# Kernel optimization log

Hardware: AMD Instinct MI355X
Metric: run time of the kernel (lower is better)

Reference implementation:

```python
import jax, jax.numpy as jnp
import numpy as np

IMG = 224
RADIUS_CUTS, AZIMUTH_CUTS = 16, 64
N_RADIUS, N_AZIMUTH = 25, 16          # kr1*kr2 = 25, ka^2 = 16
N_R = RADIUS_CUTS * N_RADIUS          # 400 sampled radii
N_A = AZIMUTH_CUTS * N_AZIMUTH        # 1024 sampled azimuths
EMBED_DIM = 96
KR, KA = 5, 4


def sample_grid(dist, H, W):
    """Per-batch polar sampling coordinates for the spherical distortion model.
    dist: (B, 4) polynomial distortion coefficients (module does dist.transpose(1,0)).
    Returns grid (B, N_R, N_A, 2) in grid_sample convention (x=width coord first),
    and theta_max (B,).
    """
    B = dist.shape[0]
    cf = 0.2 + dist.T                      # (4, B), positive odd-poly coefficients
    c = cf[:, :, None]                     # (4, B, 1) for broadcasting
    theta_max = jnp.full((B,), jnp.pi / 2, dtype=dist.dtype)

    def poly(t):                           # odd polynomial r(theta), t: (B, n)
        t2 = t * t
        return t * (c[0] + t2 * (c[1] + t2 * (c[2] + t2 * c[3])))

    # midpoint theta samples in (0, theta_max)
    theta = theta_max[:, None] * (jnp.arange(N_R, dtype=dist.dtype) + 0.5) / N_R  # (B, N_R)
    r = poly(theta) / poly(theta_max[:, None]) * (H * 0.5)                        # (B, N_R) pixels from center

    phi = (2.0 * jnp.pi) * (jnp.arange(N_A, dtype=dist.dtype) + 0.5) / N_A        # (N_A,)
    xc = r[:, :, None] * jnp.cos(phi)      # (B, N_R, N_A)
    yc = r[:, :, None] * jnp.sin(phi)
    # module: out = cat((yc/(W//2), xc/(H//2)), dim=3)
    grid = jnp.stack([yc / (W // 2), xc / (H // 2)], axis=-1)
    return grid, theta_max


def grid_sample_bilinear(img, grid):
    """torch.nn.functional.grid_sample, bilinear, align_corners=True, zeros padding.
    img: (B,C,H,W), grid: (B,Ho,Wo,2) with grid[...,0]=x (width), grid[...,1]=y (height).
    """
    B, C, H, W = img.shape
    gx = (grid[..., 0] + 1.0) * 0.5 * (W - 1)   # align_corners=True mapping
    gy = (grid[..., 1] + 1.0) * 0.5 * (H - 1)
    x0 = jnp.floor(gx); y0 = jnp.floor(gy)
    wx1 = gx - x0; wx0 = 1.0 - wx1
    wy1 = gy - y0; wy0 = 1.0 - wy1

    def corner(xi, yi, w):
        valid = (xi >= 0) & (xi <= W - 1) & (yi >= 0) & (yi <= H - 1)
        xc_ = jnp.clip(xi, 0, W - 1).astype(jnp.int32)
        yc_ = jnp.clip(yi, 0, H - 1).astype(jnp.int32)
        v = jax.vmap(lambda im, yy, xx: im[:, yy, xx])(img, yc_, xc_)  # (B,C,Ho,Wo)
        return v * (w * valid)[:, None, :, :]

    return (corner(x0, y0, wx0 * wy0) + corner(x0 + 1, y0, wx1 * wy0)
            + corner(x0, y0 + 1, wx0 * wy1) + corner(x0 + 1, y0 + 1, wx1 * wy1))


def conv2d(x, w, b, stride):
    y = jax.lax.conv_general_dilated(x, w, window_strides=stride, padding='VALID',
                                     dimension_numbers=('NCHW', 'OIHW', 'NCHW'))
    return y + b[None, :, None, None]


def setup_inputs() -> dict:
    key = jax.random.key(0)
    k = jax.random.split(key, 6)
    x = jax.random.uniform(k[0], (32, 3, IMG, IMG), dtype=jnp.float32)
    dist = jax.random.uniform(k[1], (32, 4), dtype=jnp.float32)
    w1 = jax.random.normal(k[2], (EMBED_DIM, 3, KR, KA), dtype=jnp.float32) * 0.05
    b1 = jnp.zeros((EMBED_DIM,), dtype=jnp.float32)
    w2 = jax.random.normal(k[3], (EMBED_DIM, EMBED_DIM, KR, KA), dtype=jnp.float32) * 0.05
    b2 = jnp.zeros((EMBED_DIM,), dtype=jnp.float32)
    return {"x": x, "dist": dist, "w1": w1, "b1": b1, "w2": w2, "b2": b2}


def reference(x, dist, w1, b1, w2, b2):
    B, C, H, W = x.shape
    grid, theta_max = sample_grid(dist, H, W)          # (B,400,1024,2)
    sampled = grid_sample_bilinear(x, grid)            # (B,3,400,1024)
    t = conv2d(sampled, w1, b1, (KR, KA))              # (B,96,80,256)
    t = conv2d(t, w2, b2, (KR, KA))                    # (B,96,16,64)
    t = t.reshape(B, EMBED_DIM, -1).transpose(0, 2, 1) # (B,1024,96)
    return (t, theta_max)
```

## Files before the change

kernel.cpp:

```cpp
#include <hip/hip_runtime.h>
#include <hip/hip_bf16.h>
#include <math.h>

#define NBATCH 32
#define IMGSZ  224
#define NR     400
#define NA     1024
#define ED     96
#define SROW   256

typedef __attribute__((ext_vector_type(8))) __bf16 bf16x8;
typedef __attribute__((ext_vector_type(8), aligned(8))) __bf16 bf16x8u;
typedef __attribute__((ext_vector_type(4), aligned(8))) __bf16 bf16x4a;
typedef __attribute__((ext_vector_type(4))) __bf16 bf16x4;
typedef __attribute__((ext_vector_type(4))) float f32x4;

union frag_u { struct { bf16x4a lo, hi; } p; bf16x8 v; };


#define PACK_N   (NBATCH*IMGSZ*IMGSZ)
#define PACK_N4  (PACK_N/4)
#define PACK_B   ((PACK_N4 + 255)/256)
#define PREP_N   (ED*ED*20 + 12*64*8 + NBATCH*NR + NA + NBATCH)
#define PREP_B   ((PREP_N + 255)/256)

__global__ __launch_bounds__(256)
void prep_pack_kernel(const float* __restrict__ x,
                      const float* __restrict__ dist,
                      const float* __restrict__ w1,
                      const float* __restrict__ w2,
                      __bf16* __restrict__ xp,
                      float* __restrict__ rtab,
                      float* __restrict__ costab,
                      float* __restrict__ sintab,
                      __bf16* __restrict__ w2f,
                      __bf16* __restrict__ w1f,
                      float* __restrict__ theta_out) {
    const float PI = 3.14159265358979323846f;
    const float SC = 223.0f / 224.0f;
    int bid = blockIdx.x;

    if (bid < PACK_B) {
        int i4 = bid*256 + threadIdx.x;
        if (i4 >= PACK_N4) return;
        int idx = i4 * 4;
        int b  = idx / (IMGSZ*IMGSZ);
        int px = idx - b*(IMGSZ*IMGSZ);
        const float* p = x + (size_t)b*3*IMGSZ*IMGSZ + px;
        f32x4 cr = *(const f32x4*)(p);
        f32x4 cg = *(const f32x4*)(p + IMGSZ*IMGSZ);
        f32x4 cb = *(const f32x4*)(p + 2*IMGSZ*IMGSZ);
        bf16x8 o0, o1;
        o0[0] = (__bf16)cr[0]; o0[1] = (__bf16)cg[0]; o0[2] = (__bf16)cb[0]; o0[3] = (__bf16)0.0f;
        o0[4] = (__bf16)cr[1]; o0[5] = (__bf16)cg[1]; o0[6] = (__bf16)cb[1]; o0[7] = (__bf16)0.0f;
        o1[0] = (__bf16)cr[2]; o1[1] = (__bf16)cg[2]; o1[2] = (__bf16)cb[2]; o1[3] = (__bf16)0.0f;
        o1[4] = (__bf16)cr[3]; o1[5] = (__bf16)cg[3]; o1[6] = (__bf16)cb[3]; o1[7] = (__bf16)0.0f;
        *(bf16x8*)(xp + (size_t)idx*4)     = o0;
        *(bf16x8*)(xp + (size_t)idx*4 + 8) = o1;
        return;
    }

    int idx = (bid - PACK_B)*256 + threadIdx.x;
    if (idx < ED*ED*20) {
        int j    = idx & 7;
        int lane = (idx >> 3) & 63;
        int grp  = idx >> 9;
        int nt   = grp % 6;
        int t    = grp / 6;
        int icb  = t % 3;
        int p    = t / 3;
        int sw   = (((p & 3) + icb) & 1) * 4;
        int oc = nt*16 + (lane & 15);
        int ic = icb*32 + (lane >> 4)*8 + (j ^ sw);
        w2f[idx] = (__bf16)w2[((size_t)(oc*ED + ic)*5 + (p >> 2))*4 + (p & 3)];
    } else if (idx < ED*ED*20 + 12*64*8) {
        int i2   = idx - ED*ED*20;
        int j    = i2 & 7;
        int lane = (i2 >> 3) & 63;
        int grp  = i2 >> 9;
        int ks = grp / 6, ot = grp % 6;
        int oc = ot*16 + (lane & 15);
        int k  = ks*32 + (lane >> 4)*8 + j;
        w1f[i2] = (k < 60) ? (__bf16)w1[oc*60 + k] : (__bf16)0.0f;
    } else if (idx < ED*ED*20 + 12*64*8 + NBATCH*NR) {
        int i2 = idx - ED*ED*20 - 12*64*8;
        int b = i2 / NR, i = i2 % NR;
        float c0 = 0.2f + dist[b*4+0];
        float c1 = 0.2f + dist[b*4+1];
        float c2 = 0.2f + dist[b*4+2];
        float c3 = 0.2f + dist[b*4+3];
        float tmax = 0.5f * PI;
        float t  = tmax * ((float)i + 0.5f) / (float)NR;
        float t2 = t * t;
        float pt = t * (c0 + t2*(c1 + t2*(c2 + t2*c3)));
        float tm2 = tmax * tmax;
        float pm = tmax * (c0 + tm2*(c1 + tm2*(c2 + tm2*c3)));
        rtab[i2] = pt / pm * (0.5f * (float)IMGSZ);
    } else if (idx < ED*ED*20 + 12*64*8 + NBATCH*NR + NA) {
        int j = idx - ED*ED*20 - 12*64*8 - NBATCH*NR;
        float phi = 2.0f * PI * ((float)j + 0.5f) / (float)NA;
        costab[j] = cosf(phi) * SC;
        sintab[j] = sinf(phi) * SC;
    } else if (idx < PREP_N) {
        theta_out[idx - (ED*ED*20 + 12*64*8 + NBATCH*NR + NA)] = 0.5f * PI;
    }
}

__global__ __launch_bounds__(256, 4)
void mega_kernel(const __bf16* __restrict__ xp,
                 const __bf16* __restrict__ w1f_g,
                 const __bf16* __restrict__ w2f,
                 const float* __restrict__ b1,
                 const float* __restrict__ b2,
                 const float* __restrict__ rtab,
                 const float* __restrict__ costab,
                 const float* __restrict__ sintab,
                 float* __restrict__ out) {
    __shared__ __attribute__((aligned(16))) char smem[39936];
    __bf16* s_samp0 = (__bf16*)smem;
    __bf16* s_samp1 = (__bf16*)(smem + 7680);
    __bf16* t1f     = (__bf16*)(smem + 15360);
    __bf16* s_w1f   = (__bf16*)(smem + 27648);
    float*  red     = (float*)smem;

    int tid = threadIdx.x;
    int bid = blockIdx.x;
    int r2 = bid & 15;
    int aq = (bid >> 4) & 3;
    int b  = bid >> 6;
    int wave = tid >> 6, lane = tid & 63, l15 = lane & 15, quad = lane >> 4;

    #pragma unroll
    for (int i = 0; i < 3; ++i)
        *(bf16x8*)(s_w1f + i*2048 + tid*8) = *(const bf16x8*)(w1f_g + i*2048 + tid*8);

    int col = ((lane >> 2) << 4) + wave*4 + (lane & 3);
    int az  = aq*256 + col;
    float sn = sintab[az];
    float cs = costab[az];
    int scol = wave*64 + lane;
    const __bf16* xpb = xp + (size_t)b*IMGSZ*IMGSZ*4;
    const float* rb = rtab + b*NR + r2*25;

    f32x4 acc2[6];
    #pragma unroll
    for (int nt = 0; nt < 6; ++nt) acc2[nt] = (f32x4){0.f,0.f,0.f,0.f};

    auto sample = [&](int kr, __bf16* sb) {
        #pragma unroll
        for (int q = 0; q < 5; ++q) {
            float r  = rb[kr*5 + q];
            float gx = fmaf(r, sn, 111.5f);
            float gy = fmaf(r, cs, 111.5f);
            float x0f = floorf(gx), y0f = floorf(gy);
            float wx1 = gx - x0f, wx0 = 1.0f - wx1;
            float wy1 = gy - y0f, wy0 = 1.0f - wy1;
            int ix = (int)x0f, iy = (int)y0f;
            ix = min(max(ix, 0), IMGSZ-2);
            iy = min(max(iy, 0), IMGSZ-2);
            const __bf16* img = xpb + ((size_t)iy*IMGSZ + ix)*4;
            bf16x8u p0 = *(const bf16x8u*)img;
            bf16x8u p1 = *(const bf16x8u*)(img + IMGSZ*4);
            float w00 = wy0*wx0, w01 = wy0*wx1, w10 = wy1*wx0, w11 = wy1*wx1;
            #pragma unroll
            for (int c = 0; c < 3; ++c) {
                float v = w00*(float)p0[c] + w01*(float)p0[4+c]
                        + w10*(float)p1[c] + w11*(float)p1[4+c];
                sb[(c*5 + q)*SROW + scol] = (__bf16)v;
            }
        }
    };

    sample(0, s_samp0);
    __syncthreads();

    for (int kr = 0; kr < 5; ++kr) {
        __bf16* sb = (kr & 1) ? s_samp1 : s_samp0;

        int cb = wave*64 + l15*4;
        f32x4 acc1[6];
        #pragma unroll
        for (int ot = 0; ot < 6; ++ot) acc1[ot] = (f32x4){0.f,0.f,0.f,0.f};

        frag_u fa, fb;
        fa.p.lo = *(const bf16x4a*)&sb[(quad*2    )*SROW + cb];
        fa.p.hi = *(const bf16x4a*)&sb[(quad*2 + 1)*SROW + cb];
        fb.p.lo = *(const bf16x4a*)&sb[(8 + quad*2)*SROW + cb];
        if (quad == 3) fb.p.hi = (bf16x4a){};
        else           fb.p.hi = *(const bf16x4a*)&sb[(9 + quad*2)*SROW + cb];

        #pragma unroll
        for (int ot = 0; ot < 6; ++ot) {
            bf16x8 wf0 = *(const bf16x8*)(s_w1f + (ot     )*512 + lane*8);
            bf16x8 wf1 = *(const bf16x8*)(s_w1f + (6 + ot )*512 + lane*8);
            acc1[ot] = __builtin_amdgcn_mfma_f32_16x16x32_bf16(wf0, fa.v, acc1[ot], 0, 0, 0);
            acc1[ot] = __builtin_amdgcn_mfma_f32_16x16x32_bf16(wf1, fb.v, acc1[ot], 0, 0, 0);
        }

        #pragma unroll
        for (int ot = 0; ot < 6; ++ot) {
            f32x4 v = acc1[ot] + *(const f32x4*)(b1 + ot*16 + quad*4);
            bf16x4a wv;
            wv[0] = (__bf16)v[0]; wv[1] = (__bf16)v[1];
            wv[2] = (__bf16)v[2]; wv[3] = (__bf16)v[3];
            int icbase = ot*16 + quad*4;
            int kk = wave*3 + (icbase >> 5);
            int qT = (icbase >> 3) & 3;
            int jb = (icbase & 7) ^ ((kk & 1)*4);
            *(bf16x4a*)&t1f[((kk*4 + qT)*16 + l15)*8 + jb] = wv;
        }

        #pragma unroll
        for (int icb = 0; icb < 3; ++icb) {
            int kk = wave*3 + icb;
            int p  = kr*4 + wave;
            bf16x8 af = *(const bf16x8*)&t1f[(kk*64 + lane)*8];
            const __bf16* wp = w2f + (size_t)((p*3 + icb)*6)*512 + lane*8;
            #pragma unroll
            for (int nt = 0; nt < 6; ++nt) {
                bf16x8 bf = *(const bf16x8*)(wp + nt*512);
                acc2[nt] = __builtin_amdgcn_mfma_f32_16x16x32_bf16(af, bf, acc2[nt], 0, 0, 0);
            }
        }

        __builtin_amdgcn_sched_barrier(0);

        if (kr < 4) sample(kr + 1, (kr & 1) ? s_samp0 : s_samp1);
    }

    __syncthreads();
    if (wave) {
        float* rw = red + (wave - 1)*1568;
        #pragma unroll
        for (int nt = 0; nt < 6; ++nt)
            #pragma unroll
            for (int r = 0; r < 4; ++r)
                rw[(quad*4 + r)*98 + nt*16 + l15] = acc2[nt][r];
    }
    __syncthreads();
    if (wave == 0) {
        size_t ob = ((size_t)b*1024 + r2*64 + aq*16)*ED;
        #pragma unroll
        for (int nt = 0; nt < 6; ++nt) {
            int oc = nt*16 + l15;
            float bias = b2[oc];
            #pragma unroll
            for (int r = 0; r < 4; ++r) {
                int row = quad*4 + r;
                float v = acc2[nt][r] + bias
                        + red[row*98 + oc]
                        + red[1568 + row*98 + oc]
                        + red[3136 + row*98 + oc];
                out[ob + (size_t)row*ED + oc] = v;
            }
        }
    }
}

extern "C" void kernel_launch(void* const* d_in, const int* in_sizes, int n_in,
                              void* d_out, int out_size, void* d_ws, size_t ws_size,
                              hipStream_t stream) {
    const float* x    = (const float*)d_in[0];
    const float* dist = (const float*)d_in[1];
    const float* w1   = (const float*)d_in[2];
    const float* b1   = (const float*)d_in[3];
    const float* w2   = (const float*)d_in[4];
    const float* b2   = (const float*)d_in[5];
    float* out = (float*)d_out;

    float* rtab   = (float*)d_ws;
    float* costab = rtab + NBATCH*NR;
    float* sintab = costab + NA;
    __bf16* w2f   = (__bf16*)(sintab + NA);
    __bf16* w1f   = w2f + ED*ED*20;
    __bf16* xp    = w1f + 12*64*8;

    float* theta_out = out + (size_t)NBATCH*1024*ED;

    prep_pack_kernel<<<PACK_B + PREP_B, 256, 0, stream>>>(
        x, dist, w1, w2, xp, rtab, costab, sintab, w2f, w1f, theta_out);
    mega_kernel<<<NBATCH*16*4, 256, 0, stream>>>(
        xp, w1f, w2f, b1, b2, rtab, costab, sintab, out);
}
```

Baseline: 140.5 us.

## Prefetch next bilinear gathers into registers and drop double-buffered sample LDS

Splits bilinear sampling into an issue phase that loads the image corners into registers and a finish phase that interpolates and writes to LDS. The global gathers for the next kernel row are issued before the conv2 MFMA loop so their latency overlaps with compute. The sample buffer becomes single-buffered, shrinking shared memory. The trade-off is more live registers (ten 16-byte vectors per thread), which may cause spills or lower occupancy. Reusing one buffer without an added barrier between the fragment reads and the next writes also risks a cross-wave race on the sample tile.

```diff
diff --git a/kernel.cpp b/kernel.cpp
--- a/kernel.cpp
+++ b/kernel.cpp
@@ -116,12 +116,11 @@
                  const float* __restrict__ costab,
                  const float* __restrict__ sintab,
                  float* __restrict__ out) {
-    __shared__ __attribute__((aligned(16))) char smem[39936];
-    __bf16* s_samp0 = (__bf16*)smem;
-    __bf16* s_samp1 = (__bf16*)(smem + 7680);
-    __bf16* t1f     = (__bf16*)(smem + 15360);
-    __bf16* s_w1f   = (__bf16*)(smem + 27648);
-    float*  red     = (float*)smem;
+    __shared__ __attribute__((aligned(16))) char smem[32256];
+    __bf16* s_samp = (__bf16*)smem;
+    __bf16* t1f    = (__bf16*)(smem + 7680);
+    __bf16* s_w1f  = (__bf16*)(smem + 19968);
+    float*  red    = (float*)smem;
 
     int tid = threadIdx.x;
     int bid = blockIdx.x;
@@ -146,7 +145,24 @@
     #pragma unroll
     for (int nt = 0; nt < 6; ++nt) acc2[nt] = (f32x4){0.f,0.f,0.f,0.f};
 
-    auto sample = [&](int kr, __bf16* sb) {
+    bf16x8u ga[5], gb[5];
+
+    auto sample_issue = [&](int kr) {
+        #pragma unroll
+        for (int q = 0; q < 5; ++q) {
+            float r  = rb[kr*5 + q];
+            float gx = fmaf(r, sn, 111.5f);
+            float gy = fmaf(r, cs, 111.5f);
+            int ix = (int)floorf(gx), iy = (int)floorf(gy);
+            ix = min(max(ix, 0), IMGSZ-2);
+            iy = min(max(iy, 0), IMGSZ-2);
+            const __bf16* img = xpb + ((size_t)iy*IMGSZ + ix)*4;
+            ga[q] = *(const bf16x8u*)img;
+            gb[q] = *(const bf16x8u*)(img + IMGSZ*4);
+        }
+    };
+
+    auto sample_finish = [&](int kr) {
         #pragma unroll
         for (int q = 0; q < 5; ++q) {
             float r  = rb[kr*5 + q];
@@ -155,39 +171,32 @@
             float x0f = floorf(gx), y0f = floorf(gy);
             float wx1 = gx - x0f, wx0 = 1.0f - wx1;
             float wy1 = gy - y0f, wy0 = 1.0f - wy1;
-            int ix = (int)x0f, iy = (int)y0f;
-            ix = min(max(ix, 0), IMGSZ-2);
-            iy = min(max(iy, 0), IMGSZ-2);
-            const __bf16* img = xpb + ((size_t)iy*IMGSZ + ix)*4;
-            bf16x8u p0 = *(const bf16x8u*)img;
-            bf16x8u p1 = *(const bf16x8u*)(img + IMGSZ*4);
             float w00 = wy0*wx0, w01 = wy0*wx1, w10 = wy1*wx0, w11 = wy1*wx1;
             #pragma unroll
             for (int c = 0; c < 3; ++c) {
-                float v = w00*(float)p0[c] + w01*(float)p0[4+c]
-                        + w10*(float)p1[c] + w11*(float)p1[4+c];
-                sb[(c*5 + q)*SROW + scol] = (__bf16)v;
+                float v = w00*(float)ga[q][c] + w01*(float)ga[q][4+c]
+                        + w10*(float)gb[q][c] + w11*(float)gb[q][4+c];
+                s_samp[(c*5 + q)*SROW + scol] = (__bf16)v;
             }
         }
     };
 
-    sample(0, s_samp0);
+    sample_issue(0);
+    sample_finish(0);
     __syncthreads();
 
     for (int kr = 0; kr < 5; ++kr) {
-        __bf16* sb = (kr & 1) ? s_samp1 : s_samp0;
-
         int cb = wave*64 + l15*4;
         f32x4 acc1[6];
         #pragma unroll
         for (int ot = 0; ot < 6; ++ot) acc1[ot] = (f32x4){0.f,0.f,0.f,0.f};
 
         frag_u fa, fb;
-        fa.p.lo = *(const bf16x4a*)&sb[(quad*2    )*SROW + cb];
-        fa.p.hi = *(const bf16x4a*)&sb[(quad*2 + 1)*SROW + cb];
-        fb.p.lo = *(const bf16x4a*)&sb[(8 + quad*2)*SROW + cb];
+        fa.p.lo = *(const bf16x4a*)&s_samp[(quad*2    )*SROW + cb];
+        fa.p.hi = *(const bf16x4a*)&s_samp[(quad*2 + 1)*SROW + cb];
+        fb.p.lo = *(const bf16x4a*)&s_samp[(8 + quad*2)*SROW + cb];
         if (quad == 3) fb.p.hi = (bf16x4a){};
-        else           fb.p.hi = *(const bf16x4a*)&sb[(9 + quad*2)*SROW + cb];
+        else           fb.p.hi = *(const bf16x4a*)&s_samp[(9 + quad*2)*SROW + cb];
 
         #pragma unroll
         for (int ot = 0; ot < 6; ++ot) {
@@ -210,6 +219,9 @@
             *(bf16x4a*)&t1f[((kk*4 + qT)*16 + l15)*8 + jb] = wv;
         }
 
+        if (kr < 4) sample_issue(kr + 1);
+        __builtin_amdgcn_sched_barrier(0);
+
         #pragma unroll
         for (int icb = 0; icb < 3; ++icb) {
             int kk = wave*3 + icb;
@@ -223,9 +235,7 @@
             }
         }
 
-        __builtin_amdgcn_sched_barrier(0);
-
-        if (kr < 4) sample(kr + 1, (kr & 1) ? s_samp0 : s_samp1);
+        if (kr < 4) sample_finish(kr + 1);
     }
 
     __syncthreads();
```

New measurement: 140.5 us. No clear change (-0.0%).
